# Optimization experiments

Hardware: AMD Instinct MI355X
Metric: run time of the kernel (lower is better)

The kernel has to match this reference:

```python
import jax, jax.numpy as jnp
import numpy as np

B, L, D, H = 2, 4096, 512, 8
HD = D // H  # head_dim = 64


def setup_inputs() -> dict:
    key = jax.random.key(0)
    ks = jax.random.split(key, 5)
    s = 0.02
    return {
        "x": jax.random.normal(ks[0], (B, L, D), dtype=jnp.float32),
        "w_qkv": jax.random.normal(ks[1], (D, 3 * D), dtype=jnp.float32) * s,
        "b_qkv": jax.random.normal(ks[2], (3 * D,), dtype=jnp.float32) * s,
        "w_o": jax.random.normal(ks[3], (D, D), dtype=jnp.float32) * s,
        "b_o": jax.random.normal(ks[4], (D,), dtype=jnp.float32) * s,
    }


def reference(x, w_qkv, b_qkv, w_o, b_o):
    b, l, _ = x.shape
    # QKV projection, then split heads: [B, L, 3D] -> [B, H, L, 3*HD]
    qkv = x @ w_qkv + b_qkv
    qkv = qkv.reshape(b, l, H, 3 * HD).transpose(0, 2, 1, 3)
    q, k, v = jnp.split(qkv, 3, axis=-1)  # each [B, H, L, HD]
    scale = 1.0 / jnp.sqrt(jnp.asarray(HD, dtype=q.dtype))
    # full score matrix [B, H, L, L], softmax in float32 (matches .float() cast)
    scores = jnp.einsum('bhld,bhsd->bhls', q, k) * scale
    attn = jax.nn.softmax(scores.astype(jnp.float32), axis=-1).astype(q.dtype)
    values = jnp.einsum('bhls,bhsd->bhld', attn, v)  # [B, H, L, HD]
    values = values.transpose(0, 2, 1, 3).reshape(b, l, D)
    return values @ w_o + b_o
```

## Files before the change

kernel.cpp:

```cpp
#include <hip/hip_runtime.h>


#define B_  2
#define L_  4096
#define D_  512
#define H_  8
#define HD_ 64
#define BH_ (B_*H_)
#define M_  (B_*L_)
#define QKVN (3*D_)
#define HEADSZ (BH_*L_*HD_)

typedef unsigned short ushort;
typedef unsigned int uint;
typedef __bf16 bf16x8 __attribute__((ext_vector_type(8)));
typedef float  f32x4  __attribute__((ext_vector_type(4)));
typedef float  f32x16 __attribute__((ext_vector_type(16)));

typedef const __attribute__((address_space(1))) void g_void;
typedef __attribute__((address_space(3))) void l_void;

#define C2_ 0.18033688011112042f

#if __has_builtin(__builtin_amdgcn_exp2f)
#define FEXP2(x) __builtin_amdgcn_exp2f(x)
#else
#define FEXP2(x) exp2f(x)
#endif

__device__ __forceinline__ ushort f2bf(float f) {
    __bf16 h = (__bf16)f;
    return __builtin_bit_cast(ushort, h);
}

__device__ __forceinline__ uint pack2(float lo, float hi) {
    return (uint)f2bf(lo) | ((uint)f2bf(hi) << 16);
}

__global__ __launch_bounds__(256)
void prep_k(const float* __restrict__ x, ushort* __restrict__ xb,
            const float* __restrict__ wq, ushort* __restrict__ wtq,
            const float* __restrict__ wo, ushort* __restrict__ wto)
{
    int bid = blockIdx.x, tid = threadIdx.x;
    if (bid < 4096) {
        int idx = bid * 256 + tid;
        float4 v = ((const float4*)x)[idx];
        ushort4 o; o.x = f2bf(v.x); o.y = f2bf(v.y); o.z = f2bf(v.z); o.w = f2bf(v.w);
        ((ushort4*)xb)[idx] = o;
    } else if (bid < 7168) {
        int idx = (bid - 4096) * 256 + tid;
        int c = idx / D_, r = idx % D_;
        wtq[idx] = f2bf(wq[r * QKVN + c]);
    } else {
        int idx = (bid - 7168) * 256 + tid;
        int c = idx / D_, r = idx % D_;
        wto[idx] = f2bf(wo[r * D_ + c]);
    }
}

template<int BN>
__global__ __launch_bounds__(256)
void gemm_bt(const ushort* __restrict__ A, const ushort* __restrict__ Bt,
             const float* __restrict__ bias, void* __restrict__ out,
             int M, int N, int K, int mode)
{
    constexpr int MT = (BN == 128) ? 4 : 2;
    constexpr int BL = BN / 64;
    __shared__ ushort As[2][128 * 32];
    __shared__ ushort Bs[2][BN * 32];

    const int tid  = threadIdx.x;
    const int lane = tid & 63;
    const int wid  = tid >> 6;
    const int wm   = (BN == 128) ? (wid >> 1) : wid;
    const int wn   = (BN == 128) ? (wid & 1) : 0;
    const int lr   = lane & 15;
    const int quad = lane >> 4;
    const int tm = blockIdx.x, tn = blockIdx.y;

    f32x4 acc[MT][4] = {};
    const int arow = tm * 128;
    const int brow = tn * BN;

    auto STAGE = [&](int t) {
        const int k0 = t * 32;
        ushort* as = &As[t & 1][0];
        ushort* bs = &Bs[t & 1][0];
        #pragma unroll
        for (int i = 0; i < 2; i++) {
            int c   = i * 256 + tid;
            int row = c >> 2;
            int kk  = (c & 3) * 8;
            __builtin_amdgcn_global_load_lds(
                (g_void*)&A[(size_t)(arow + row) * K + k0 + kk],
                (l_void*)&as[c * 8], 16, 0, 0);
        }
        #pragma unroll
        for (int i = 0; i < BL; i++) {
            int c   = i * 256 + tid;
            int row = c >> 2;
            int kk  = (c & 3) * 8;
            __builtin_amdgcn_global_load_lds(
                (g_void*)&Bt[(size_t)(brow + row) * K + k0 + kk],
                (l_void*)&bs[c * 8], 16, 0, 0);
        }
    };

    const int NK = K / 32;
    STAGE(0);
    for (int t = 0; t < NK; t++) {
        __syncthreads();
        if (t + 1 < NK) STAGE(t + 1);
        const ushort* as = &As[t & 1][0];
        const ushort* bs = &Bs[t & 1][0];

        bf16x8 af[MT], bfr[4];
        #pragma unroll
        for (int mt = 0; mt < MT; mt++)
            af[mt] = *(const bf16x8*)&as[(wm * (MT * 16) + mt * 16 + lr) * 32 + quad * 8];
        #pragma unroll
        for (int nt = 0; nt < 4; nt++)
            bfr[nt] = *(const bf16x8*)&bs[(wn * 64 + nt * 16 + lr) * 32 + quad * 8];
        #pragma unroll
        for (int mt = 0; mt < MT; mt++)
            #pragma unroll
            for (int nt = 0; nt < 4; nt++)
                acc[mt][nt] = __builtin_amdgcn_mfma_f32_16x16x32_bf16(
                    af[mt], bfr[nt], acc[mt][nt], 0, 0, 0);
    }

    if (mode == 0) {
        #pragma unroll
        for (int nt = 0; nt < 4; nt++) {
            int col = tn * BN + wn * 64 + nt * 16 + lr;
            float bv = bias[col];
            #pragma unroll
            for (int mt = 0; mt < MT; mt++) {
                #pragma unroll
                for (int r = 0; r < 4; r++) {
                    int row = tm * 128 + wm * (MT * 16) + mt * 16 + quad * 4 + r;
                    ((float*)out)[(size_t)row * N + col] = acc[mt][nt][r] + bv;
                }
            }
        }
    } else {
        const int g     = (tn * BN + wn * 64) >> 6;
        const int which = g % 3;
        const int h     = g / 3;
        ushort* qkv = (ushort*)out;
        if (which != 2) {
            const float qscale = (which == 0) ? C2_ : 1.0f;
            #pragma unroll
            for (int nt = 0; nt < 4; nt++) {
                int d = nt * 16 + lr;
                float bv = bias[g * 64 + d];
                #pragma unroll
                for (int mt = 0; mt < MT; mt++) {
                    #pragma unroll
                    for (int r = 0; r < 4; r++) {
                        int row = tm * 128 + wm * (MT * 16) + mt * 16 + quad * 4 + r;
                        int b = row >> 12;
                        int l = row & (L_ - 1);
                        float v = (acc[mt][nt][r] + bv) * qscale;
                        qkv[which * HEADSZ + (((b * H_ + h) * L_ + l) * HD_) + d]
                            = f2bf(v);
                    }
                }
            }
        } else {
            ushort* vt = qkv + 2 * HEADSZ;
            #pragma unroll
            for (int nt = 0; nt < 4; nt++) {
                int d = nt * 16 + lr;
                float bv = bias[g * 64 + d];
                #pragma unroll
                for (int mt = 0; mt < MT; mt++) {
                    int row0 = tm * 128 + wm * (MT * 16) + mt * 16 + quad * 4;
                    int b = row0 >> 12;
                    int l = row0 & (L_ - 1);
                    ushort4 pk;
                    pk.x = f2bf(acc[mt][nt][0] + bv);
                    pk.y = f2bf(acc[mt][nt][1] + bv);
                    pk.z = f2bf(acc[mt][nt][2] + bv);
                    pk.w = f2bf(acc[mt][nt][3] + bv);
                    *(ushort4*)&vt[((size_t)(b * H_ + h) * HD_ + d) * L_ + l] = pk;
                }
            }
        }
    }
}

__global__ __launch_bounds__(256)
void attn_k(const ushort* __restrict__ Q, const ushort* __restrict__ K,
            const ushort* __restrict__ VT, ushort* __restrict__ O)
{
    __shared__ __align__(16) ushort Ksm[2][64 * 64];
    __shared__ __align__(16) ushort Vsm[4][64 * 64];

    const int tid  = threadIdx.x;
    const int lane = tid & 63;
    const int wid  = tid >> 6;
    const int l31  = lane & 31;
    const int hi   = lane >> 5;

    const int wg  = blockIdx.x;
    const int xcd = wg & 7, sl = wg >> 3;
    const int bh  = (xcd << 1) | (sl >> 5);
    const int q0  = (sl & 31) * 128;
    const size_t base = (size_t)bh * (L_ * HD_);

    const int sr0 = tid >> 3,        sr1 = (tid + 256) >> 3;
    const int sc0 = ((tid & 7) ^ (sr0 & 7)) * 8;
    const int sc1 = ((tid & 7) ^ (sr1 & 7)) * 8;
    const ushort* Kg0 = K  + base + sr0 * HD_ + sc0;
    const ushort* Kg1 = K  + base + sr1 * HD_ + sc1;
    const ushort* Vg0 = VT + base + (size_t)sr0 * L_ + sc0;
    const ushort* Vg1 = VT + base + (size_t)sr1 * L_ + sc1;

    bf16x8 qf[4];
    {
        const ushort* qp = Q + base + (size_t)(q0 + wid * 32 + l31) * HD_ + hi * 8;
        #pragma unroll
        for (int ks = 0; ks < 4; ks++) qf[ks] = *(const bf16x8*)(qp + ks * 16);
    }

    const int swz = (l31 & 7) << 4;
    int cbe[4];
    #pragma unroll
    for (int ks = 0; ks < 4; ks++) cbe[ks] = ((ks * 32 + hi * 16) ^ swz) >> 1;
    const int kr0 = l31 * 64, kr1 = (32 + l31) * 64;

    const f32x16 Z = {};
    bf16x8 onesB;
    #pragma unroll
    for (int i = 0; i < 8; i++) onesB[i] = (__bf16)1.0f;

    f32x16 o0 = {}, o1 = {}, l_acc = {};
    f32x16 sEA, sEB, sOA, sOB;

    auto STAGE = [&](int tt) {
        const size_t ko = (size_t)tt * 64 * HD_;
        const int    vo = tt * 64;
        ushort* kb = &Ksm[tt & 1][0];
        ushort* vb = &Vsm[tt & 3][0];
        __builtin_amdgcn_global_load_lds((g_void*)(Kg0 + ko), (l_void*)(kb + tid * 8),        16, 0, 0);
        __builtin_amdgcn_global_load_lds((g_void*)(Kg1 + ko), (l_void*)(kb + tid * 8 + 2048), 16, 0, 0);
        __builtin_amdgcn_global_load_lds((g_void*)(Vg0 + vo), (l_void*)(vb + tid * 8),        16, 0, 0);
        __builtin_amdgcn_global_load_lds((g_void*)(Vg1 + vo), (l_void*)(vb + tid * 8 + 2048), 16, 0, 0);
    };

    auto QK = [&](int tt, f32x16& SA, f32x16& SB) {
        const ushort* kb = &Ksm[tt & 1][0];
        {
            bf16x8 k0 = *(const bf16x8*)&kb[kr0 + cbe[0]];
            bf16x8 k1 = *(const bf16x8*)&kb[kr1 + cbe[0]];
            SA = __builtin_amdgcn_mfma_f32_32x32x16_bf16(k0, qf[0], Z, 0, 0, 0);
            SB = __builtin_amdgcn_mfma_f32_32x32x16_bf16(k1, qf[0], Z, 0, 0, 0);
        }
        #pragma unroll
        for (int ks = 1; ks < 4; ks++) {
            bf16x8 k0 = *(const bf16x8*)&kb[kr0 + cbe[ks]];
            bf16x8 k1 = *(const bf16x8*)&kb[kr1 + cbe[ks]];
            SA = __builtin_amdgcn_mfma_f32_32x32x16_bf16(k0, qf[ks], SA, 0, 0, 0);
            SB = __builtin_amdgcn_mfma_f32_32x32x16_bf16(k1, qf[ks], SB, 0, 0, 0);
        }
    };

    auto SMPV = [&](int tp, f32x16& SA, f32x16& SB) {
        const ushort* vb = &Vsm[tp & 3][0];
        #pragma unroll
        for (int i = 0; i < 16; i++) { SA[i] = FEXP2(SA[i]); SB[i] = FEXP2(SB[i]); }
        #pragma unroll
        for (int ks = 0; ks < 4; ks++) {
            const f32x16& P = (ks >> 1) ? SB : SA;
            const int r0 = 8 * (ks & 1);
            uint a0 = pack2(P[r0 + 0], P[r0 + 1]);
            uint a1 = pack2(P[r0 + 2], P[r0 + 3]);
            uint b0 = pack2(P[r0 + 4], P[r0 + 5]);
            uint b1 = pack2(P[r0 + 6], P[r0 + 7]);
            asm("v_permlane32_swap_b32 %0, %1" : "+v"(a0), "+v"(b0));
            asm("v_permlane32_swap_b32 %0, %1" : "+v"(a1), "+v"(b1));
            uint4 w; w.x = a0; w.y = a1; w.z = b0; w.w = b1;
            bf16x8 pa = __builtin_bit_cast(bf16x8, w);
            bf16x8 v0 = *(const bf16x8*)&vb[kr0 + cbe[ks]];
            bf16x8 v1 = *(const bf16x8*)&vb[kr1 + cbe[ks]];
            o0 = __builtin_amdgcn_mfma_f32_32x32x16_bf16(pa, v0, o0, 0, 0, 0);
            o1 = __builtin_amdgcn_mfma_f32_32x32x16_bf16(pa, v1, o1, 0, 0, 0);
            l_acc = __builtin_amdgcn_mfma_f32_32x32x16_bf16(pa, onesB, l_acc, 0, 0, 0);
        }
    };

    STAGE(0);

    for (int t = 0; t < L_ / 64; t += 2) {
        __syncthreads();
        STAGE(t + 1);
        QK(t, sEA, sEB);
        if (t > 0) SMPV(t - 1, sOA, sOB);
        __syncthreads();
        if (t + 2 < L_ / 64) STAGE(t + 2);
        QK(t + 1, sOA, sOB);
        SMPV(t, sEA, sEB);
    }
    SMPV(L_ / 64 - 1, sOA, sOB);

    const int b = bh >> 3, h = bh & 7;
    #pragma unroll
    for (int r = 0; r < 16; r++) {
        const int qrl = (r & 3) + 8 * (r >> 2) + 4 * hi;
        const float inv = 1.0f / l_acc[r];
        const size_t row = (size_t)(b * L_ + q0 + wid * 32 + qrl) * D_ + h * HD_ + l31;
        O[row]      = f2bf(o0[r] * inv);
        O[row + 32] = f2bf(o1[r] * inv);
    }
}

extern "C" void kernel_launch(void* const* d_in, const int* in_sizes, int n_in,
                              void* d_out, int out_size, void* d_ws, size_t ws_size,
                              hipStream_t stream)
{
    const float* x     = (const float*)d_in[0];
    const float* w_qkv = (const float*)d_in[1];
    const float* b_qkv = (const float*)d_in[2];
    const float* w_o   = (const float*)d_in[3];
    const float* b_o   = (const float*)d_in[4];

    char* ws = (char*)d_ws;
    size_t o = 0;
    ushort* xb   = (ushort*)(ws + o); o += (size_t)M_ * D_ * 2;
    ushort* qkv  = (ushort*)(ws + o); o += (size_t)3 * HEADSZ * 2;
    ushort* attn = (ushort*)(ws + o); o += (size_t)M_ * D_ * 2;
    ushort* wtq  = (ushort*)(ws + o); o += (size_t)QKVN * D_ * 2;
    ushort* wto  = (ushort*)(ws + o);

    hipLaunchKernelGGL(prep_k, dim3(8192), dim3(256), 0, stream,
                       x, xb, w_qkv, wtq, w_o, wto);
    hipLaunchKernelGGL((gemm_bt<128>), dim3(M_ / 128, QKVN / 128), dim3(256), 0, stream,
                       xb, wtq, b_qkv, (void*)qkv, M_, QKVN, D_, 1);
    hipLaunchKernelGGL(attn_k, dim3(512), dim3(256), 0, stream,
                       qkv, qkv + HEADSZ, qkv + 2 * HEADSZ, attn);
    hipLaunchKernelGGL((gemm_bt<64>), dim3(M_ / 128, D_ / 64), dim3(256), 0, stream,
                       attn, wto, b_o, d_out, M_, D_, D_, 0);
}
```

Baseline: 209.7 us.

## Split attention KV tile across two wave groups with LDS reduction

Doubles the attention workgroup to 512 threads. Each group of four waves takes half of every 64-key tile (32 keys) for the same 128 queries, and the partial outputs and row sums are combined through shared memory at the end. Per-wave register pressure drops (one score accumulator instead of two), and each wave issues half the staging loads. This is meant to raise occupancy and latency hiding, at the cost of a final LDS reduction, extra barriers and duplicated Q fragments per wave.

```diff
diff --git a/kernel.cpp b/kernel.cpp
--- a/kernel.cpp
+++ b/kernel.cpp
@@ -191,16 +191,19 @@
     }
 }
 
-__global__ __launch_bounds__(256)
+__global__ __launch_bounds__(512, 4)
 void attn_k(const ushort* __restrict__ Q, const ushort* __restrict__ K,
             const ushort* __restrict__ VT, ushort* __restrict__ O)
 {
-    __shared__ __align__(16) ushort Ksm[2][64 * 64];
-    __shared__ __align__(16) ushort Vsm[4][64 * 64];
+    __shared__ __align__(16) ushort SMEM[24576];
+    ushort* Ksm = SMEM;
+    ushort* Vsm = SMEM + 8192;
 
     const int tid  = threadIdx.x;
     const int lane = tid & 63;
     const int wid  = tid >> 6;
+    const int qw   = wid & 3;
+    const int kh   = wid >> 2;
     const int l31  = lane & 31;
     const int hi   = lane >> 5;
 
@@ -210,17 +213,14 @@
     const int q0  = (sl & 31) * 128;
     const size_t base = (size_t)bh * (L_ * HD_);
 
-    const int sr0 = tid >> 3,        sr1 = (tid + 256) >> 3;
-    const int sc0 = ((tid & 7) ^ (sr0 & 7)) * 8;
-    const int sc1 = ((tid & 7) ^ (sr1 & 7)) * 8;
-    const ushort* Kg0 = K  + base + sr0 * HD_ + sc0;
-    const ushort* Kg1 = K  + base + sr1 * HD_ + sc1;
-    const ushort* Vg0 = VT + base + (size_t)sr0 * L_ + sc0;
-    const ushort* Vg1 = VT + base + (size_t)sr1 * L_ + sc1;
+    const int sr = tid >> 3;
+    const int sc = ((tid & 7) ^ (sr & 7)) * 8;
+    const ushort* Kg = K  + base + sr * HD_ + sc;
+    const ushort* Vg = VT + base + (size_t)sr * L_ + sc;
 
     bf16x8 qf[4];
     {
-        const ushort* qp = Q + base + (size_t)(q0 + wid * 32 + l31) * HD_ + hi * 8;
+        const ushort* qp = Q + base + (size_t)(q0 + qw * 32 + l31) * HD_ + hi * 8;
         #pragma unroll
         for (int ks = 0; ks < 4; ks++) qf[ks] = *(const bf16x8*)(qp + ks * 16);
     }
@@ -229,7 +229,8 @@
     int cbe[4];
     #pragma unroll
     for (int ks = 0; ks < 4; ks++) cbe[ks] = ((ks * 32 + hi * 16) ^ swz) >> 1;
-    const int kr0 = l31 * 64, kr1 = (32 + l31) * 64;
+    const int krW  = (kh * 32 + l31) * 64;
+    const int kr0v = l31 * 64, kr1v = (32 + l31) * 64;
 
     const f32x16 Z = {};
     bf16x8 onesB;
@@ -237,54 +238,48 @@
     for (int i = 0; i < 8; i++) onesB[i] = (__bf16)1.0f;
 
     f32x16 o0 = {}, o1 = {}, l_acc = {};
-    f32x16 sEA, sEB, sOA, sOB;
+    f32x16 sE, sO;
 
     auto STAGE = [&](int tt) {
-        const size_t ko = (size_t)tt * 64 * HD_;
-        const int    vo = tt * 64;
-        ushort* kb = &Ksm[tt & 1][0];
-        ushort* vb = &Vsm[tt & 3][0];
-        __builtin_amdgcn_global_load_lds((g_void*)(Kg0 + ko), (l_void*)(kb + tid * 8),        16, 0, 0);
-        __builtin_amdgcn_global_load_lds((g_void*)(Kg1 + ko), (l_void*)(kb + tid * 8 + 2048), 16, 0, 0);
-        __builtin_amdgcn_global_load_lds((g_void*)(Vg0 + vo), (l_void*)(vb + tid * 8),        16, 0, 0);
-        __builtin_amdgcn_global_load_lds((g_void*)(Vg1 + vo), (l_void*)(vb + tid * 8 + 2048), 16, 0, 0);
+        __builtin_amdgcn_global_load_lds(
+            (g_void*)(Kg + (size_t)tt * 64 * HD_),
+            (l_void*)(Ksm + (tt & 1) * 4096 + tid * 8), 16, 0, 0);
+        __builtin_amdgcn_global_load_lds(
+            (g_void*)(Vg + tt * 64),
+            (l_void*)(Vsm + (tt & 3) * 4096 + tid * 8), 16, 0, 0);
     };
 
-    auto QK = [&](int tt, f32x16& SA, f32x16& SB) {
-        const ushort* kb = &Ksm[tt & 1][0];
+    auto QK = [&](int tt, f32x16& S) {
+        const ushort* kb = Ksm + (tt & 1) * 4096;
         {
-            bf16x8 k0 = *(const bf16x8*)&kb[kr0 + cbe[0]];
-            bf16x8 k1 = *(const bf16x8*)&kb[kr1 + cbe[0]];
-            SA = __builtin_amdgcn_mfma_f32_32x32x16_bf16(k0, qf[0], Z, 0, 0, 0);
-            SB = __builtin_amdgcn_mfma_f32_32x32x16_bf16(k1, qf[0], Z, 0, 0, 0);
+            bf16x8 k0 = *(const bf16x8*)&kb[krW + cbe[0]];
+            S = __builtin_amdgcn_mfma_f32_32x32x16_bf16(k0, qf[0], Z, 0, 0, 0);
         }
         #pragma unroll
         for (int ks = 1; ks < 4; ks++) {
-            bf16x8 k0 = *(const bf16x8*)&kb[kr0 + cbe[ks]];
-            bf16x8 k1 = *(const bf16x8*)&kb[kr1 + cbe[ks]];
-            SA = __builtin_amdgcn_mfma_f32_32x32x16_bf16(k0, qf[ks], SA, 0, 0, 0);
-            SB = __builtin_amdgcn_mfma_f32_32x32x16_bf16(k1, qf[ks], SB, 0, 0, 0);
+            bf16x8 k0 = *(const bf16x8*)&kb[krW + cbe[ks]];
+            S = __builtin_amdgcn_mfma_f32_32x32x16_bf16(k0, qf[ks], S, 0, 0, 0);
         }
     };
 
-    auto SMPV = [&](int tp, f32x16& SA, f32x16& SB) {
-        const ushort* vb = &Vsm[tp & 3][0];
-        #pragma unroll
-        for (int i = 0; i < 16; i++) { SA[i] = FEXP2(SA[i]); SB[i] = FEXP2(SB[i]); }
-        #pragma unroll
-        for (int ks = 0; ks < 4; ks++) {
-            const f32x16& P = (ks >> 1) ? SB : SA;
-            const int r0 = 8 * (ks & 1);
-            uint a0 = pack2(P[r0 + 0], P[r0 + 1]);
-            uint a1 = pack2(P[r0 + 2], P[r0 + 3]);
-            uint b0 = pack2(P[r0 + 4], P[r0 + 5]);
-            uint b1 = pack2(P[r0 + 6], P[r0 + 7]);
+    auto SMPV = [&](int tp, f32x16& S) {
+        const ushort* vb = Vsm + (tp & 3) * 4096;
+        #pragma unroll
+        for (int i = 0; i < 16; i++) S[i] = FEXP2(S[i]);
+        #pragma unroll
+        for (int kk = 0; kk < 2; kk++) {
+            const int ks = kh * 2 + kk;
+            const int r0 = 8 * kk;
+            uint a0 = pack2(S[r0 + 0], S[r0 + 1]);
+            uint a1 = pack2(S[r0 + 2], S[r0 + 3]);
+            uint b0 = pack2(S[r0 + 4], S[r0 + 5]);
+            uint b1 = pack2(S[r0 + 6], S[r0 + 7]);
             asm("v_permlane32_swap_b32 %0, %1" : "+v"(a0), "+v"(b0));
             asm("v_permlane32_swap_b32 %0, %1" : "+v"(a1), "+v"(b1));
             uint4 w; w.x = a0; w.y = a1; w.z = b0; w.w = b1;
             bf16x8 pa = __builtin_bit_cast(bf16x8, w);
-            bf16x8 v0 = *(const bf16x8*)&vb[kr0 + cbe[ks]];
-            bf16x8 v1 = *(const bf16x8*)&vb[kr1 + cbe[ks]];
+            bf16x8 v0 = *(const bf16x8*)&vb[kr0v + cbe[ks]];
+            bf16x8 v1 = *(const bf16x8*)&vb[kr1v + cbe[ks]];
             o0 = __builtin_amdgcn_mfma_f32_32x32x16_bf16(pa, v0, o0, 0, 0, 0);
             o1 = __builtin_amdgcn_mfma_f32_32x32x16_bf16(pa, v1, o1, 0, 0, 0);
             l_acc = __builtin_amdgcn_mfma_f32_32x32x16_bf16(pa, onesB, l_acc, 0, 0, 0);
@@ -296,23 +291,40 @@
     for (int t = 0; t < L_ / 64; t += 2) {
         __syncthreads();
         STAGE(t + 1);
-        QK(t, sEA, sEB);
-        if (t > 0) SMPV(t - 1, sOA, sOB);
+        QK(t, sE);
+        if (t > 0) SMPV(t - 1, sO);
         __syncthreads();
         if (t + 2 < L_ / 64) STAGE(t + 2);
-        QK(t + 1, sOA, sOB);
-        SMPV(t, sEA, sEB);
-    }
-    SMPV(L_ / 64 - 1, sOA, sOB);
-
-    const int b = bh >> 3, h = bh & 7;
-    #pragma unroll
-    for (int r = 0; r < 16; r++) {
-        const int qrl = (r & 3) + 8 * (r >> 2) + 4 * hi;
-        const float inv = 1.0f / l_acc[r];
-        const size_t row = (size_t)(b * L_ + q0 + wid * 32 + qrl) * D_ + h * HD_ + l31;
-        O[row]      = f2bf(o0[r] * inv);
-        O[row + 32] = f2bf(o1[r] * inv);
+        QK(t + 1, sO);
+        SMPV(t, sE);
+    }
+    SMPV(L_ / 64 - 1, sO);
+
+    __syncthreads();
+    float* red = (float*)SMEM;
+    if (kh == 1) {
+        float* p = red + (qw * 64 + lane) * 48;
+        #pragma unroll
+        for (int r = 0; r < 16; r++) {
+            p[r] = o0[r]; p[16 + r] = o1[r]; p[32 + r] = l_acc[r];
+        }
+    }
+    __syncthreads();
+    if (kh == 0) {
+        const float* p = red + (qw * 64 + lane) * 48;
+        #pragma unroll
+        for (int r = 0; r < 16; r++) {
+            o0[r] += p[r]; o1[r] += p[16 + r]; l_acc[r] += p[32 + r];
+        }
+        const int b = bh >> 3, h = bh & 7;
+        #pragma unroll
+        for (int r = 0; r < 16; r++) {
+            const int qrl = (r & 3) + 8 * (r >> 2) + 4 * hi;
+            const float inv = 1.0f / l_acc[r];
+            const size_t row = (size_t)(b * L_ + q0 + qw * 32 + qrl) * D_ + h * HD_ + l31;
+            O[row]      = f2bf(o0[r] * inv);
+            O[row + 32] = f2bf(o1[r] * inv);
+        }
     }
 }
 
@@ -338,7 +350,7 @@
                        x, xb, w_qkv, wtq, w_o, wto);
     hipLaunchKernelGGL((gemm_bt<128>), dim3(M_ / 128, QKVN / 128), dim3(256), 0, stream,
                        xb, wtq, b_qkv, (void*)qkv, M_, QKVN, D_, 1);
-    hipLaunchKernelGGL(attn_k, dim3(512), dim3(256), 0, stream,
+    hipLaunchKernelGGL(attn_k, dim3(512), dim3(512), 0, stream,
                        qkv, qkv + HEADSZ, qkv + 2 * HEADSZ, attn);
     hipLaunchKernelGGL((gemm_bt<64>), dim3(M_ / 128, D_ / 64), dim3(256), 0, stream,
                        attn, wto, b_o, d_out, M_, D_, D_, 0);
```

Measured after the change: 204.3 us, median of 2. -2.6%, faster.
